# Performance work log

Hardware: AMD Instinct MI355X
Metric: run time of the kernel (lower is better)

Reference implementation:

```python
import jax, jax.numpy as jnp
import numpy as np
from jax import lax

DIM, DIN, NST, DTR, K = 96, 192, 16, 6, 4
B, H, W = 2, 56, 56
MID, SEMID = 24, 24
EPS = 1e-5


def _ln(x, g, b):
    m = x.mean(-1, keepdims=True)
    v = ((x - m) ** 2).mean(-1, keepdims=True)
    return (x - m) / jnp.sqrt(v + EPS) * g + b


def _bn(x, g, b, m, v):  # eval-mode BatchNorm2d, NCHW
    return (x - m[None, :, None, None]) / jnp.sqrt(v[None, :, None, None] + EPS) * g[None, :, None, None] + b[None, :, None, None]


def _conv(x, w, pad, groups=1):
    return lax.conv_general_dilated(x, w, (1, 1), [(pad, pad), (pad, pad)],
                                    dimension_numbers=('NCHW', 'OIHW', 'NCHW'),
                                    feature_group_count=groups)


def _vssm(xn, in_proj_w, conv_w, conv_b, x_proj_w, dt_proj_w, dt_proj_b,
          A_log, Ds, out_norm_g, out_norm_b, out_proj_w):
    Bz, Hh, Ww, C = xn.shape
    L = Hh * Ww
    xz = xn @ in_proj_w.T                      # (B,H,W,2*Din)
    xc, z = jnp.split(xz, 2, axis=-1)
    xc = xc.transpose(0, 3, 1, 2)              # (B,Din,H,W)
    xc = _conv(xc, conv_w, pad=1, groups=DIN) + conv_b[None, :, None, None]
    xc = jax.nn.silu(xc)
    # 4 scan directions: row-major, col-major, and their reverses
    x1 = xc.reshape(Bz, DIN, L)
    x2 = xc.transpose(0, 1, 3, 2).reshape(Bz, DIN, L)
    xs = jnp.stack([x1, x2], axis=1)
    xs = jnp.concatenate([xs, jnp.flip(xs, axis=-1)], axis=1)   # (B,4,Din,L)
    x_dbl = jnp.einsum('bkdl,kcd->bkcl', xs, x_proj_w)          # (B,4,dtR+2N,L)
    dts, Bs, Cs = jnp.split(x_dbl, [DTR, DTR + NST], axis=2)
    delta = jax.nn.softplus(jnp.einsum('bkrl,kdr->bkdl', dts, dt_proj_w)
                            + dt_proj_b[None, :, :, None])      # (B,4,Din,L)
    A = -jnp.exp(A_log).reshape(K, DIN, NST)
    dA = jnp.exp(jnp.einsum('bkdl,kdn->bkdln', delta, A))       # (B,4,Din,L,N)
    dBu = jnp.einsum('bkdl,bknl,bkdl->bkdln', delta, Bs, xs)

    def comb(c1, c2):
        a1, b1 = c1
        a2, b2 = c2
        return (a1 * a2, a2 * b1 + b2)

    _, hs = lax.associative_scan(comb, (dA, dBu), axis=3)       # h_t = dA_t h_{t-1} + dBu_t
    ys = jnp.einsum('bkdln,bknl->bkdl', hs, Cs) + Ds.reshape(1, K, DIN, 1) * xs
    inv = jnp.flip(ys[:, 2:4], axis=-1)

    def t_back(y):
        return y.reshape(Bz, DIN, Ww, Hh).transpose(0, 1, 3, 2).reshape(Bz, DIN, L)

    y = ys[:, 0] + t_back(ys[:, 1]) + inv[:, 0] + t_back(inv[:, 1])
    y = y.reshape(Bz, DIN, Hh, Ww).transpose(0, 2, 3, 1)        # (B,H,W,Din)
    y = _ln(y, out_norm_g, out_norm_b) * jax.nn.silu(z)
    return y @ out_proj_w.T                                      # (B,H,W,dim)


def setup_inputs() -> dict:
    key = jax.random.key(0)
    ks = jax.random.split(key, 16)
    r = lambda k, s, sc=0.05: (jax.random.normal(k, s, dtype=jnp.float32) * sc)
    d = {}
    d['x'] = jax.random.normal(ks[0], (B, DIM, H, W), dtype=jnp.float32)
    d['norm1_g'] = jnp.ones((DIM,), jnp.float32); d['norm1_b'] = jnp.zeros((DIM,), jnp.float32)
    d['in_proj_w'] = r(ks[1], (2 * DIN, DIM))
    d['conv_w'] = r(ks[2], (DIN, 1, 3, 3), 0.2); d['conv_b'] = jnp.zeros((DIN,), jnp.float32)
    d['x_proj_w'] = r(ks[3], (K, DTR + 2 * NST, DIN))
    d['dt_proj_w'] = r(ks[4], (K, DIN, DTR), 0.2)
    d['dt_proj_b'] = jnp.full((K, DIN), -2.0, jnp.float32)
    d['A_log'] = jnp.log(jnp.broadcast_to(jnp.arange(1, NST + 1, dtype=jnp.float32), (K * DIN, NST)) + 0.0)
    d['Ds'] = jnp.ones((K * DIN,), jnp.float32)
    d['out_norm_g'] = jnp.ones((DIN,), jnp.float32); d['out_norm_b'] = jnp.zeros((DIN,), jnp.float32)
    d['out_proj_w'] = r(ks[5], (DIM, DIN))
    d['scale1'] = jnp.full((DIM,), 0.1, jnp.float32)
    d['norm2_g'] = jnp.ones((DIM,), jnp.float32); d['norm2_b'] = jnp.zeros((DIM,), jnp.float32)
    d['lc_w1'] = r(ks[6], (MID, DIM, 1, 1), 0.1)
    d['lc_g1'] = jnp.ones((MID,), jnp.float32); d['lc_b1'] = jnp.zeros((MID,), jnp.float32)
    d['lc_m1'] = jnp.zeros((MID,), jnp.float32); d['lc_v1'] = jnp.ones((MID,), jnp.float32)
    d['lc_w2'] = r(ks[7], (MID, MID, 3, 3), 0.1)
    d['lc_g2'] = jnp.ones((MID,), jnp.float32); d['lc_b2'] = jnp.zeros((MID,), jnp.float32)
    d['lc_m2'] = jnp.zeros((MID,), jnp.float32); d['lc_v2'] = jnp.ones((MID,), jnp.float32)
    d['lc_w3'] = r(ks[8], (DIM, MID, 1, 1), 0.1)
    d['lc_g3'] = jnp.ones((DIM,), jnp.float32); d['lc_b3'] = jnp.zeros((DIM,), jnp.float32)
    d['lc_m3'] = jnp.zeros((DIM,), jnp.float32); d['lc_v3'] = jnp.ones((DIM,), jnp.float32)
    d['se_w1'] = r(ks[9], (SEMID, DIM), 0.1)
    d['se_w2'] = r(ks[10], (DIM, SEMID), 0.1)
    d['scale2'] = jnp.full((DIM,), 0.1, jnp.float32)
    return d


def reference(x, norm1_g, norm1_b, in_proj_w, conv_w, conv_b, x_proj_w, dt_proj_w,
              dt_proj_b, A_log, Ds, out_norm_g, out_norm_b, out_proj_w, scale1,
              norm2_g, norm2_b, lc_w1, lc_g1, lc_b1, lc_m1, lc_v1, lc_w2, lc_g2,
              lc_b2, lc_m2, lc_v2, lc_w3, lc_g3, lc_b3, lc_m3, lc_v3, se_w1,
              se_w2, scale2):
    x_hwc = x.transpose(0, 2, 3, 1)                    # (B,H,W,C)
    vl = _vssm(_ln(x_hwc, norm1_g, norm1_b), in_proj_w, conv_w, conv_b,
               x_proj_w, dt_proj_w, dt_proj_b, A_log, Ds,
               out_norm_g, out_norm_b, out_proj_w)
    vl = vl + scale1 * x_hwc                           # scaled residual
    vb = _ln(vl, norm2_g, norm2_b).transpose(0, 3, 1, 2)  # (B,C,H,W)
    h = jax.nn.relu(_bn(_conv(vb, lc_w1, pad=0), lc_g1, lc_b1, lc_m1, lc_v1))
    h = jax.nn.relu(_bn(_conv(h, lc_w2, pad=1), lc_g2, lc_b2, lc_m2, lc_v2))
    h = _bn(_conv(h, lc_w3, pad=0), lc_g3, lc_b3, lc_m3, lc_v3)
    # SE channel attention
    w = h.mean(axis=(2, 3))                            # (B,C)
    w = jax.nn.sigmoid(jax.nn.relu(w @ se_w1.T) @ se_w2.T)
    h = h * w[:, :, None, None]
    return h + scale2[None, :, None, None] * vl.transpose(0, 3, 1, 2)
```

## Files before the change

kernel.cpp:

```cpp
#include <hip/hip_runtime.h>
#include <math.h>

#define DIMC 96
#define DINC 192
#define NSTC 16
#define DTRC 6
#define KDIR 4
#define BB   2
#define HH   56
#define WWD  56
#define LL   3136
#define NPIX (BB*LL)
#define EPSF 1e-5f
#define NCH  98
#define LC   32
#define NCHAIN (BB*KDIR*DINC)
#define NCOLS 152

#define OFF_XCRAW  0u
#define OFF_XCONV  1204224u
#define OFF_ZS     2408448u
#define OFF_DTS    3612672u
#define OFF_BCB    3763200u
#define OFF_BCC    4164608u
#define OFF_XSCANT 4566016u
#define OFF_CUMD   6974464u
#define OFF_YS     11791360u
#define OFF_HENDT  0u
#define OFF_SUMDT  16608256u
#define OFF_VL     6974464u
#define OFF_H1     7576576u
#define OFF_H2     7727104u
#define OFF_H3     7877632u
#define OFF_POOL   8479744u
#define OFF_SEW    8479936u

__device__ __forceinline__ float siluf(float x) { return x / (1.f + __expf(-x)); }
__device__ __forceinline__ float softplusf(float x) {
    return fmaxf(x, 0.f) + __logf(1.f + __expf(-fabsf(x)));
}
__device__ __forceinline__ float fexp2(float x) {
#if __has_builtin(__builtin_amdgcn_exp2f)
    return __builtin_amdgcn_exp2f(x);
#else
    return exp2f(x);
#endif
}
#define LOG2E 1.44269504088896f

__global__ __launch_bounds__(256) void gemm1_k(const float* __restrict__ x,
                                               const float* __restrict__ g,
                                               const float* __restrict__ bt,
                                               const float* __restrict__ W,
                                               float* __restrict__ xcr,
                                               float* __restrict__ zs) {
    __shared__ float xT[64 * 97];
    __shared__ float wT[96 * 100];
    __shared__ float mA[64], iA[64];
    int row0 = blockIdx.x * 64;
    int b = row0 / LL, pos0 = row0 % LL;
    int c0 = blockIdx.y * 96;
    for (int f = threadIdx.x; f < 96 * 16; f += 256) {
        int ch = f >> 4, po = (f & 15) * 4;
        float4 v = *(const float4*)&x[((size_t)b * DIMC + ch) * LL + pos0 + po];
        xT[(po + 0) * 97 + ch] = v.x; xT[(po + 1) * 97 + ch] = v.y;
        xT[(po + 2) * 97 + ch] = v.z; xT[(po + 3) * 97 + ch] = v.w;
    }
    for (int f = threadIdx.x; f < 96 * 24; f += 256) {
        int r = f / 24, kq = (f % 24) * 4;
        *(float4*)&wT[r * 100 + kq] = *(const float4*)&W[(size_t)(c0 + r) * DIMC + kq];
    }
    __syncthreads();
    if (threadIdx.x < 64) {
        float s = 0.f, q = 0.f;
        const float* xr = &xT[threadIdx.x * 97];
        for (int c = 0; c < 96; ++c) { float v = xr[c]; s += v; q = fmaf(v, v, q); }
        float m = s * (1.f / 96.f);
        mA[threadIdx.x] = m;
        iA[threadIdx.x] = rsqrtf(q * (1.f / 96.f) - m * m + EPSF);
    }
    __syncthreads();
    for (int e = threadIdx.x; e < 64 * 96; e += 256) {
        int row = e / 96, col = e - row * 96;
        float v = xT[row * 97 + col];
        xT[row * 97 + col] = (v - mA[row]) * iA[row] * g[col] + bt[col];
    }
    __syncthreads();
    int tc = threadIdx.x & 15, tr = threadIdx.x >> 4;
    float acc[4][6] = {};
    for (int k = 0; k < 96; ++k) {
        float xv[4], wv[6];
#pragma unroll
        for (int i = 0; i < 4; ++i) xv[i] = xT[(4 * tr + i) * 97 + k];
#pragma unroll
        for (int j = 0; j < 6; ++j) wv[j] = wT[(tc + 16 * j) * 100 + k];
#pragma unroll
        for (int i = 0; i < 4; ++i)
#pragma unroll
            for (int j = 0; j < 6; ++j) acc[i][j] = fmaf(xv[i], wv[j], acc[i][j]);
    }
    int pos = pos0 + 4 * tr;
    if (c0 < DINC) {
#pragma unroll
        for (int j = 0; j < 6; ++j) {
            int col = c0 + tc + 16 * j;
            float4 v = make_float4(acc[0][j], acc[1][j], acc[2][j], acc[3][j]);
            *(float4*)&xcr[((size_t)b * DINC + col) * LL + pos] = v;
        }
    } else {
#pragma unroll
        for (int i = 0; i < 4; ++i)
#pragma unroll
            for (int j = 0; j < 6; ++j) {
                int zc = c0 - DINC + tc + 16 * j;
                zs[(size_t)(row0 + 4 * tr + i) * DINC + zc] = siluf(acc[i][j]);
            }
    }
}

__global__ __launch_bounds__(448) void dwconv_k(const float* __restrict__ xcr,
                                                const float* __restrict__ cw,
                                                const float* __restrict__ cb,
                                                float* __restrict__ xconv) {
    __shared__ float P[56 * 57];
    int bd = blockIdx.x;
    int d = bd % DINC;
    size_t base = (size_t)bd * LL;
    for (int t = threadIdx.x; t < LL; t += 448)
        P[(t / 56) * 57 + (t % 56)] = xcr[base + t];
    float wk[9];
#pragma unroll
    for (int q = 0; q < 9; ++q) wk[q] = cw[d * 9 + q];
    float bias = cb[d];
    __syncthreads();
    for (int t = threadIdx.x; t < LL; t += 448) {
        int h = t / 56, w = t % 56;
        float acc = bias;
#pragma unroll
        for (int ky = 0; ky < 3; ++ky) {
            int y = h + ky - 1;
            if ((unsigned)y >= 56u) continue;
#pragma unroll
            for (int kx = 0; kx < 3; ++kx) {
                int xq = w + kx - 1;
                if ((unsigned)xq >= 56u) continue;
                acc = fmaf(wk[ky * 3 + kx], P[y * 57 + xq], acc);
            }
        }
        xconv[base + t] = siluf(acc);
    }
}

__global__ __launch_bounds__(256) void gemmx_k(const float* __restrict__ xconv,
                                               const float* __restrict__ xpw,
                                               float* __restrict__ dts,
                                               float* __restrict__ bcB,
                                               float* __restrict__ bcC,
                                               float* __restrict__ xscanT) {
    __shared__ float xT[32 * 49];
    __shared__ float wT[38 * 52];
    int row0 = blockIdx.x * 32;
    int b = row0 / LL, pos0 = row0 % LL;
    int by = blockIdx.y;
    int m = threadIdx.x & 31, cg = threadIdx.x >> 5;
    float acc[5] = {};
    for (int kc = 0; kc < 4; ++kc) {
        if (kc) __syncthreads();
        for (int f = threadIdx.x; f < 48 * 8; f += 256) {
            int dd = f >> 3, po = (f & 7) * 4;
            float4 v = *(const float4*)&xconv[((size_t)b * DINC + kc * 48 + dd) * LL + pos0 + po];
            xT[(po + 0) * 49 + dd] = v.x; xT[(po + 1) * 49 + dd] = v.y;
            xT[(po + 2) * 49 + dd] = v.z; xT[(po + 3) * 49 + dd] = v.w;
        }
        for (int f = threadIdx.x; f < 38 * 12; f += 256) {
            int r = f / 12, kq = (f % 12) * 4;
            *(float4*)&wT[r * 52 + kq] =
                *(const float4*)&xpw[(size_t)(by * 38 + r) * DINC + kc * 48 + kq];
        }
        __syncthreads();
#pragma unroll 4
        for (int k = 0; k < 48; ++k) {
            float xv = xT[m * 49 + k];
#pragma unroll
            for (int j = 0; j < 5; ++j) {
                int idx = cg + 8 * j;
                float wv = (idx < 38) ? wT[idx * 52 + k] : 0.f;
                acc[j] = fmaf(xv, wv, acc[j]);
            }
        }
        if (by == 0) {
            for (int f = threadIdx.x; f < 32 * 48; f += 256) {
                int i = f / 48, dd = f - 48 * (f / 48);
                float v = xT[i * 49 + dd];
                int pos = pos0 + i;
                int hh = pos / 56, w = pos - 56 * hh;
                int lt = w * 56 + hh;
                size_t bb = (size_t)b * 2;
                int col = kc * 48 + dd;
                xscanT[(bb * LL + pos) * DINC + col] = v;
                xscanT[((bb + 1) * LL + lt) * DINC + col] = v;
            }
        }
    }
    {
        int pos = pos0 + m;
        int h = pos / 56, w = pos - 56 * h;
        int lt = w * 56 + h;
        int l = (by == 0) ? pos : (by == 1) ? lt : (by == 2) ? (LL - 1 - pos) : (LL - 1 - lt);
        size_t rb = (size_t)(b * KDIR + by) * LL + l;
#pragma unroll
        for (int j = 0; j < 5; ++j) {
            int idx = cg + 8 * j;
            if (idx >= 38) continue;
            float v = acc[j];
            if (idx < DTRC)    dts[rb * DTRC + idx] = v;
            else if (idx < 22) bcB[rb * NSTC + (idx - 6)] = v;
            else               bcC[rb * NSTC + (idx - 22)] = v;
        }
    }
}

__global__ __launch_bounds__(64) void pass1_k(const float* __restrict__ dts,
                                              const float* __restrict__ bcB,
                                              const float* __restrict__ bcC,
                                              const float* __restrict__ alog,
                                              const float* __restrict__ dtw,
                                              const float* __restrict__ dtb,
                                              const float* __restrict__ xscanT,
                                              float* __restrict__ hendT,
                                              float* __restrict__ sumdT,
                                              float* __restrict__ ysT,
                                              float* __restrict__ cumdT) {
    __shared__ float sdt[LC * 7];
    __shared__ float sB[LC * 16];
    __shared__ float sC[LC * 16];
    int blk = blockIdx.x;
    int c = blk % NCH;
    int dtile = (blk / NCH) % 3;
    int bk = blk / (NCH * 3);
    int k = bk & 3, b = bk >> 2;
    int l0 = c * LC;
    int t = threadIdx.x;
    int d = dtile * 64 + t;
    const float* dsrc = dts + ((size_t)bk * LL + l0) * DTRC;
    for (int f = t; f < LC * DTRC; f += 64) sdt[(f / DTRC) * 7 + (f % DTRC)] = dsrc[f];
    const float* bB = bcB + ((size_t)bk * LL + l0) * NSTC;
    const float* bC = bcC + ((size_t)bk * LL + l0) * NSTC;
    for (int f = t; f < LC * NSTC; f += 64) { sB[f] = bB[f]; sC[f] = bC[f]; }
    float wr[DTRC];
    {
        const float* wp = dtw + ((size_t)k * DINC + d) * DTRC;
#pragma unroll
        for (int r = 0; r < DTRC; ++r) wr[r] = wp[r];
    }
    float bias = dtb[k * DINC + d];
    float An2[NSTC];
    {
        const float* ap = alog + ((size_t)(k * DINC + d)) * NSTC;
#pragma unroll
        for (int n = 0; n < NSTC; ++n) An2[n] = -__expf(ap[n]) * LOG2E;
    }
    __syncthreads();
    float h[NSTC];
#pragma unroll
    for (int n = 0; n < NSTC; ++n) h[n] = 0.f;
    float cum = 0.f;
    bool rev = (k >= 2);
    const float* xbase = xscanT + ((size_t)(b * 2 + (k & 1)) * LL) * DINC + d;
    int xi0 = rev ? (LL - 1 - l0) : l0;
    float* yrow = ysT + ((size_t)bk * LL + l0) * DINC + d;
    float* crow = cumdT + ((size_t)bk * LL + l0) * DINC + d;
#pragma unroll 8
    for (int s = 0; s < LC; ++s) {
        float acc = bias;
#pragma unroll
        for (int r = 0; r < DTRC; ++r) acc = fmaf(wr[r], sdt[s * 7 + r], acc);
        float dv = softplusf(acc);
        float xv = xbase[(size_t)(rev ? (xi0 - s) : (xi0 + s)) * DINC];
        cum += dv;
        float dx = dv * xv;
        const float4* B4 = (const float4*)&sB[s * 16];
        const float4* C4 = (const float4*)&sC[s * 16];
        float y = 0.f;
#pragma unroll
        for (int nq = 0; nq < 4; ++nq) {
            float4 Bv = B4[nq], Cv = C4[nq];
            float e0 = fexp2(An2[nq * 4 + 0] * dv);
            h[nq * 4 + 0] = fmaf(e0, h[nq * 4 + 0], dx * Bv.x);
            y = fmaf(h[nq * 4 + 0], Cv.x, y);
            float e1 = fexp2(An2[nq * 4 + 1] * dv);
            h[nq * 4 + 1] = fmaf(e1, h[nq * 4 + 1], dx * Bv.y);
            y = fmaf(h[nq * 4 + 1], Cv.y, y);
            float e2 = fexp2(An2[nq * 4 + 2] * dv);
            h[nq * 4 + 2] = fmaf(e2, h[nq * 4 + 2], dx * Bv.z);
            y = fmaf(h[nq * 4 + 2], Cv.z, y);
            float e3 = fexp2(An2[nq * 4 + 3] * dv);
            h[nq * 4 + 3] = fmaf(e3, h[nq * 4 + 3], dx * Bv.w);
            y = fmaf(h[nq * 4 + 3], Cv.w, y);
        }
        yrow[(size_t)s * DINC] = y;
        crow[(size_t)s * DINC] = cum;
    }
#pragma unroll
    for (int n = 0; n < NSTC; ++n)
        hendT[((size_t)(bk * NCH + c) * NSTC + n) * DINC + d] = h[n];
    sumdT[(size_t)(bk * NCH + c) * DINC + d] = cum;
}

__global__ __launch_bounds__(256) void scan2_k(float* __restrict__ hendT,
                                               const float* __restrict__ sumdT,
                                               const float* __restrict__ alog) {
    int gid = blockIdx.x * 256 + threadIdx.x;
    int d = gid % DINC;
    int n = (gid / DINC) % NSTC;
    int bk = gid / (DINC * NSTC);
    int k = bk & 3;
    float An2 = -__expf(alog[((size_t)(k * DINC + d)) * NSTC + n]) * LOG2E;
    float h = 0.f;
#pragma unroll 4
    for (int c = 0; c < NCH; ++c) {
        size_t idx = ((size_t)(bk * NCH + c) * NSTC + n) * DINC + d;
        float he = hendT[idx];
        float sd = sumdT[(size_t)(bk * NCH + c) * DINC + d];
        hendT[idx] = h;
        h = fmaf(fexp2(An2 * sd), h, he);
    }
}

__global__ __launch_bounds__(256) void pass2_k(const float* __restrict__ bcC,
                                               const float* __restrict__ alog,
                                               const float* __restrict__ hpreT,
                                               const float* __restrict__ cumdT,
                                               float* __restrict__ ysT) {
    __shared__ float sA2[DINC * 17];
    __shared__ float sH[DINC * 17];
    __shared__ float sC[LC * NSTC];
    int blk = blockIdx.x;
    int c = blk % NCH;
    int bk = blk / NCH;
    int k = bk & 3;
    int l0 = c * LC;
    int tid = threadIdx.x;
    const float* ap = alog + (size_t)k * DINC * NSTC;
    for (int f = tid; f < DINC * NSTC; f += 256) {
        int dq = f / NSTC, n = f % NSTC;
        sA2[dq * 17 + n] = -__expf(ap[f]) * LOG2E;
    }
    for (int f = tid; f < DINC * NSTC; f += 256) {
        int n = f / DINC, dq = f % DINC;
        sH[dq * 17 + n] = hpreT[((size_t)(bk * NCH + c) * NSTC + n) * DINC + dq];
    }
    const float* bC = bcC + ((size_t)bk * LL + l0) * NSTC;
    for (int f = tid; f < LC * NSTC; f += 256) sC[f] = bC[f];
    __syncthreads();
    for (int e = tid; e < LC * DINC; e += 256) {
        int li = e / DINC, d = e - DINC * (e / DINC);
        size_t gq = ((size_t)bk * LL + l0 + li) * DINC + d;
        float cd = cumdT[gq];
        float y = ysT[gq];
        const float* A = &sA2[d * 17];
        const float* Hp = &sH[d * 17];
        const float* Cp = &sC[li * NSTC];
#pragma unroll
        for (int n = 0; n < NSTC; ++n)
            y = fmaf(Hp[n] * fexp2(A[n] * cd), Cp[n], y);
        ysT[gq] = y;
    }
}

__global__ __launch_bounds__(256) void gemm2_k(const float* __restrict__ ysT,
                                               const float* __restrict__ xscanT,
                                               const float* __restrict__ dsv,
                                               const float* __restrict__ g,
                                               const float* __restrict__ bt,
                                               const float* __restrict__ zs,
                                               const float* __restrict__ opw,
                                               const float* __restrict__ x,
                                               const float* __restrict__ sc1,
                                               float* __restrict__ vl) {
    __shared__ float xT[16 * 193];
    __shared__ float wT[96 * 52];
    __shared__ float mA[16], iA[16];
    __shared__ float sD[DINC];
    int row0 = blockIdx.x * 16;
    int b = row0 / LL, pos0 = row0 % LL;
    if (threadIdx.x < DINC)
        sD[threadIdx.x] = dsv[threadIdx.x] + dsv[DINC + threadIdx.x] +
                          dsv[2 * DINC + threadIdx.x] + dsv[3 * DINC + threadIdx.x];
    __syncthreads();
    size_t base = (size_t)b * KDIR * LL;
    size_t xbase = (size_t)b * 2 * LL;
    for (int f = threadIdx.x; f < 16 * DINC; f += 256) {
        int r = f / DINC, d = f - DINC * (f / DINC);
        int pos = pos0 + r;
        int hh = pos / 56, w = pos - 56 * hh;
        int lt = w * 56 + hh;
        float y = ysT[(base + pos) * DINC + d]
                + ysT[(base + LL + lt) * DINC + d]
                + ysT[(base + 2 * LL + (LL - 1 - pos)) * DINC + d]
                + ysT[(base + 3 * LL + (LL - 1 - lt)) * DINC + d];
        float xv = xscanT[(xbase + pos) * DINC + d];
        xT[r * 193 + d] = fmaf(xv, sD[d], y);
    }
    __syncthreads();
    {
        int r = threadIdx.x >> 4, sc = threadIdx.x & 15;
        float s = 0.f, q = 0.f;
#pragma unroll
        for (int j = 0; j < 12; ++j) {
            float v = xT[r * 193 + sc + 16 * j];
            s += v; q = fmaf(v, v, q);
        }
        s += __shfl_xor(s, 1, 16); q += __shfl_xor(q, 1, 16);
        s += __shfl_xor(s, 2, 16); q += __shfl_xor(q, 2, 16);
        s += __shfl_xor(s, 4, 16); q += __shfl_xor(q, 4, 16);
        s += __shfl_xor(s, 8, 16); q += __shfl_xor(q, 8, 16);
        if (sc == 0) {
            float m = s * (1.f / 192.f);
            mA[r] = m;
            iA[r] = rsqrtf(q * (1.f / 192.f) - m * m + EPSF);
        }
    }
    __syncthreads();
    for (int e = threadIdx.x; e < 16 * 192; e += 256) {
        int row = e / 192, col = e - row * 192;
        float v = xT[row * 193 + col];
        float z = zs[(size_t)row0 * DINC + e];
        xT[row * 193 + col] = ((v - mA[row]) * iA[row] * g[col] + bt[col]) * z;
    }
    int tc = threadIdx.x & 15, tr = threadIdx.x >> 4;
    float acc[6] = {};
    for (int kc = 0; kc < 4; ++kc) {
        __syncthreads();
        for (int f = threadIdx.x; f < 96 * 12; f += 256) {
            int r = f / 12, kq = (f % 12) * 4;
            *(float4*)&wT[r * 52 + kq] = *(const float4*)&opw[(size_t)r * DINC + kc * 48 + kq];
        }
        __syncthreads();
#pragma unroll 4
        for (int k = 0; k < 48; ++k) {
            float xv = xT[tr * 193 + kc * 48 + k];
#pragma unroll
            for (int j = 0; j < 6; ++j) acc[j] = fmaf(xv, wT[(tc + 16 * j) * 52 + k], acc[j]);
        }
    }
    {
        int pos = pos0 + tr;
#pragma unroll
        for (int j = 0; j < 6; ++j) {
            int col = tc + 16 * j;
            float v = fmaf(sc1[col], x[((size_t)b * DIMC + col) * LL + pos], acc[j]);
            vl[(size_t)(row0 + tr) * DIMC + col] = v;
        }
    }
}

__global__ __launch_bounds__(256) void ln2conv1_k(const float* __restrict__ vl,
                                                  const float* __restrict__ g,
                                                  const float* __restrict__ bt,
                                                  const float* __restrict__ w1,
                                                  const float* __restrict__ g1,
                                                  const float* __restrict__ b1,
                                                  const float* __restrict__ m1,
                                                  const float* __restrict__ v1,
                                                  float* __restrict__ h1) {
    __shared__ float row[4][96];
    int wv = threadIdx.x >> 6, lane = threadIdx.x & 63;
    int pix = blockIdx.x * 4 + wv;
    const float* vr = vl + (size_t)pix * DIMC;
    float a0 = vr[lane];
    float a1 = (lane < 32) ? vr[64 + lane] : 0.f;
    float s = a0 + a1, q = a0 * a0 + a1 * a1;
    for (int o = 32; o; o >>= 1) { s += __shfl_xor(s, o, 64); q += __shfl_xor(q, o, 64); }
    float m = s * (1.f / 96.f);
    float inv = rsqrtf(q * (1.f / 96.f) - m * m + EPSF);
    row[wv][lane] = (a0 - m) * inv * g[lane] + bt[lane];
    if (lane < 32) row[wv][64 + lane] = (a1 - m) * inv * g[64 + lane] + bt[64 + lane];
    __syncthreads();
    if (lane < 24) {
        const float* wr = w1 + lane * 96;
        float acc = 0.f;
#pragma unroll 8
        for (int c = 0; c < 96; ++c) acc = fmaf(row[wv][c], wr[c], acc);
        float bn = (acc - m1[lane]) * rsqrtf(v1[lane] + EPSF) * g1[lane] + b1[lane];
        int b = pix / LL, pos = pix % LL;
        h1[((size_t)b * 24 + lane) * LL + pos] = fmaxf(bn, 0.f);
    }
}

__global__ __launch_bounds__(256) void conv2_k(const float* __restrict__ h1,
                                               const float* __restrict__ w2,
                                               const float* __restrict__ g2,
                                               const float* __restrict__ b2,
                                               const float* __restrict__ m2,
                                               const float* __restrict__ v2,
                                               float* __restrict__ h2) {
    int i = blockIdx.x * 256 + threadIdx.x;
    int pos = i % LL, mo = (i / LL) % 24, b = i / (LL * 24);
    int hh = pos / WWD, ww = pos % WWD;
    float acc = 0.f;
    for (int c = 0; c < 24; ++c) {
        const float* src = h1 + ((size_t)b * 24 + c) * LL;
        const float* wk = w2 + ((size_t)(mo * 24 + c)) * 9;
#pragma unroll
        for (int ky = 0; ky < 3; ++ky) {
            int y = hh + ky - 1;
            if ((unsigned)y >= HH) continue;
#pragma unroll
            for (int kx = 0; kx < 3; ++kx) {
                int xq = ww + kx - 1;
                if ((unsigned)xq >= WWD) continue;
                acc = fmaf(wk[ky * 3 + kx], src[y * WWD + xq], acc);
            }
        }
    }
    float bn = (acc - m2[mo]) * rsqrtf(v2[mo] + EPSF) * g2[mo] + b2[mo];
    h2[i] = fmaxf(bn, 0.f);
}

__global__ __launch_bounds__(256) void conv3_k(const float* __restrict__ h2,
                                               const float* __restrict__ w3,
                                               const float* __restrict__ g3,
                                               const float* __restrict__ b3,
                                               const float* __restrict__ m3,
                                               const float* __restrict__ v3,
                                               float* __restrict__ h3) {
    int i = blockIdx.x * 256 + threadIdx.x;
    int pos = i % LL, c = (i / LL) % DIMC, b = i / (LL * DIMC);
    const float* wr = w3 + c * 24;
    float acc = 0.f;
#pragma unroll
    for (int mo = 0; mo < 24; ++mo)
        acc = fmaf(wr[mo], h2[((size_t)b * 24 + mo) * LL + pos], acc);
    h3[i] = (acc - m3[c]) * rsqrtf(v3[c] + EPSF) * g3[c] + b3[c];
}

__global__ __launch_bounds__(256) void pool_k(const float* __restrict__ h3,
                                              float* __restrict__ pooled) {
    int bc = blockIdx.x;
    const float* p = h3 + (size_t)bc * LL;
    float s = 0.f;
    for (int i = threadIdx.x; i < LL; i += 256) s += p[i];
    for (int o = 32; o; o >>= 1) s += __shfl_xor(s, o, 64);
    __shared__ float wsum[4];
    if ((threadIdx.x & 63) == 0) wsum[threadIdx.x >> 6] = s;
    __syncthreads();
    if (threadIdx.x == 0) pooled[bc] = (wsum[0] + wsum[1] + wsum[2] + wsum[3]) * (1.f / 3136.f);
}

__global__ __launch_bounds__(128) void semlp_k(const float* __restrict__ pooled,
                                               const float* __restrict__ sw1,
                                               const float* __restrict__ sw2,
                                               float* __restrict__ sew) {
    __shared__ float pl[2][96];
    __shared__ float hid[2][24];
    for (int i = threadIdx.x; i < 192; i += 128) pl[i / 96][i % 96] = pooled[i];
    __syncthreads();
    if (threadIdx.x < 48) {
        int b = threadIdx.x / 24, mo = threadIdx.x % 24;
        float acc = 0.f;
        for (int c = 0; c < 96; ++c) acc = fmaf(pl[b][c], sw1[mo * 96 + c], acc);
        hid[b][mo] = fmaxf(acc, 0.f);
    }
    __syncthreads();
    for (int i = threadIdx.x; i < 192; i += 128) {
        int b = i / 96, c = i % 96;
        float acc = 0.f;
        for (int mo = 0; mo < 24; ++mo) acc = fmaf(hid[b][mo], sw2[c * 24 + mo], acc);
        sew[i] = 1.f / (1.f + __expf(-acc));
    }
}

__global__ __launch_bounds__(256) void final_k(const float* __restrict__ h3,
                                               const float* __restrict__ sew,
                                               const float* __restrict__ vl,
                                               const float* __restrict__ sc2,
                                               float* __restrict__ out) {
    int i = blockIdx.x * 256 + threadIdx.x;
    int pos = i % LL, c = (i / LL) % DIMC, b = i / (LL * DIMC);
    out[i] = fmaf(h3[i], sew[b * DIMC + c],
                  sc2[c] * vl[((size_t)b * LL + pos) * DIMC + c]);
}

extern "C" void kernel_launch(void* const* d_in, const int* in_sizes, int n_in,
                              void* d_out, int out_size, void* d_ws, size_t ws_size,
                              hipStream_t stream) {
    const float* x    = (const float*)d_in[0];
    const float* n1g  = (const float*)d_in[1];
    const float* n1b  = (const float*)d_in[2];
    const float* ipw  = (const float*)d_in[3];
    const float* cw   = (const float*)d_in[4];
    const float* cb   = (const float*)d_in[5];
    const float* xpw  = (const float*)d_in[6];
    const float* dtw  = (const float*)d_in[7];
    const float* dtb  = (const float*)d_in[8];
    const float* alog = (const float*)d_in[9];
    const float* dsv  = (const float*)d_in[10];
    const float* ong  = (const float*)d_in[11];
    const float* onb  = (const float*)d_in[12];
    const float* opw  = (const float*)d_in[13];
    const float* sc1  = (const float*)d_in[14];
    const float* n2g  = (const float*)d_in[15];
    const float* n2b  = (const float*)d_in[16];
    const float* w1   = (const float*)d_in[17];
    const float* g1   = (const float*)d_in[18];
    const float* b1   = (const float*)d_in[19];
    const float* m1   = (const float*)d_in[20];
    const float* v1   = (const float*)d_in[21];
    const float* w2   = (const float*)d_in[22];
    const float* g2   = (const float*)d_in[23];
    const float* b2   = (const float*)d_in[24];
    const float* m2   = (const float*)d_in[25];
    const float* v2   = (const float*)d_in[26];
    const float* w3   = (const float*)d_in[27];
    const float* g3   = (const float*)d_in[28];
    const float* b3   = (const float*)d_in[29];
    const float* m3   = (const float*)d_in[30];
    const float* v3   = (const float*)d_in[31];
    const float* sw1  = (const float*)d_in[32];
    const float* sw2  = (const float*)d_in[33];
    const float* sc2  = (const float*)d_in[34];
    float* ws = (float*)d_ws;
    float* out = (float*)d_out;

    gemm1_k<<<dim3(NPIX / 64, 4), 256, 0, stream>>>(x, n1g, n1b, ipw,
                                                    ws + OFF_XCRAW, ws + OFF_ZS);
    dwconv_k<<<BB * DINC, 448, 0, stream>>>(ws + OFF_XCRAW, cw, cb, ws + OFF_XCONV);
    gemmx_k<<<dim3(NPIX / 32, 4), 256, 0, stream>>>(ws + OFF_XCONV, xpw, ws + OFF_DTS,
                                                    ws + OFF_BCB, ws + OFF_BCC, ws + OFF_XSCANT);

    pass1_k<<<BB * KDIR * 3 * NCH, 64, 0, stream>>>(
        ws + OFF_DTS, ws + OFF_BCB, ws + OFF_BCC, alog, dtw, dtb,
        ws + OFF_XSCANT, ws + OFF_HENDT, ws + OFF_SUMDT, ws + OFF_YS, ws + OFF_CUMD);
    scan2_k<<<(NCHAIN * NSTC) / 256, 256, 0, stream>>>(ws + OFF_HENDT, ws + OFF_SUMDT, alog);
    pass2_k<<<BB * KDIR * NCH, 256, 0, stream>>>(
        ws + OFF_BCC, alog, ws + OFF_HENDT, ws + OFF_CUMD, ws + OFF_YS);

    gemm2_k<<<NPIX / 16, 256, 0, stream>>>(ws + OFF_YS, ws + OFF_XSCANT, dsv,
                                           ong, onb, ws + OFF_ZS, opw, x, sc1, ws + OFF_VL);
    ln2conv1_k<<<NPIX / 4, 256, 0, stream>>>(ws + OFF_VL, n2g, n2b, w1, g1, b1, m1, v1,
                                             ws + OFF_H1);
    conv2_k<<<(BB * 24 * LL) / 256, 256, 0, stream>>>(ws + OFF_H1, w2, g2, b2, m2, v2,
                                                      ws + OFF_H2);
    conv3_k<<<(BB * DIMC * LL) / 256, 256, 0, stream>>>(ws + OFF_H2, w3, g3, b3, m3, v3,
                                                        ws + OFF_H3);
    pool_k<<<BB * DIMC, 256, 0, stream>>>(ws + OFF_H3, ws + OFF_POOL);
    semlp_k<<<1, 128, 0, stream>>>(ws + OFF_POOL, sw1, sw2, ws + OFF_SEW);
    final_k<<<(BB * DIMC * LL) / 256, 256, 0, stream>>>(ws + OFF_H3, ws + OFF_SEW, ws + OFF_VL,
                                                        sc2, out);
    (void)in_sizes; (void)n_in; (void)out_size; (void)ws_size;
}
```

Before: 218.6 us.

## Halve scan chunk length and retile in_proj GEMM to 32-row blocks

Changes the selective-scan chunking from 98 chunks of 32 to 196 chunks of 16 and moves the chunk-end state buffers to new workspace offsets. The first GEMM now processes 32 rows per block with one row per thread and 12 output columns, does the LayerNorm statistics with all threads plus shuffle reductions, and stages the z output through shared memory so its global writes are coalesced. The aim is more parallelism in the scan and fewer serial steps per chunk, plus better load balance and coalescing in the GEMM. The cost is more chunk-boundary state traffic, a longer inter-chunk carry scan, and a GEMM with less register-level reuse of loaded operands.

```diff
diff --git a/kernel.cpp b/kernel.cpp
--- a/kernel.cpp
+++ b/kernel.cpp
@@ -12,8 +12,8 @@
 #define LL   3136
 #define NPIX (BB*LL)
 #define EPSF 1e-5f
-#define NCH  98
-#define LC   32
+#define NCH  196
+#define LC   16
 #define NCHAIN (BB*KDIR*DINC)
 #define NCOLS 152
 
@@ -26,8 +26,8 @@
 #define OFF_XSCANT 4566016u
 #define OFF_CUMD   6974464u
 #define OFF_YS     11791360u
-#define OFF_HENDT  0u
-#define OFF_SUMDT  16608256u
+#define OFF_HENDT  16608256u
+#define OFF_SUMDT  21425152u
 #define OFF_VL     6974464u
 #define OFF_H1     7576576u
 #define OFF_H2     7727104u
@@ -54,14 +54,15 @@
                                                const float* __restrict__ W,
                                                float* __restrict__ xcr,
                                                float* __restrict__ zs) {
-    __shared__ float xT[64 * 97];
+    __shared__ float xT[32 * 97];
     __shared__ float wT[96 * 100];
-    __shared__ float mA[64], iA[64];
-    int row0 = blockIdx.x * 64;
+    __shared__ float mA[32], iA[32];
+    int row0 = blockIdx.x * 32;
     int b = row0 / LL, pos0 = row0 % LL;
-    int c0 = blockIdx.y * 96;
-    for (int f = threadIdx.x; f < 96 * 16; f += 256) {
-        int ch = f >> 4, po = (f & 15) * 4;
+    int by = blockIdx.y;
+    int c0 = by * 96;
+    for (int f = threadIdx.x; f < 96 * 8; f += 256) {
+        int ch = f >> 3, po = (f & 7) * 4;
         float4 v = *(const float4*)&x[((size_t)b * DIMC + ch) * LL + pos0 + po];
         xT[(po + 0) * 97 + ch] = v.x; xT[(po + 1) * 97 + ch] = v.y;
         xT[(po + 2) * 97 + ch] = v.z; xT[(po + 3) * 97 + ch] = v.w;
@@ -71,50 +72,53 @@
         *(float4*)&wT[r * 100 + kq] = *(const float4*)&W[(size_t)(c0 + r) * DIMC + kq];
     }
     __syncthreads();
-    if (threadIdx.x < 64) {
+    {
+        int r = threadIdx.x >> 3, sc = threadIdx.x & 7;
         float s = 0.f, q = 0.f;
-        const float* xr = &xT[threadIdx.x * 97];
-        for (int c = 0; c < 96; ++c) { float v = xr[c]; s += v; q = fmaf(v, v, q); }
-        float m = s * (1.f / 96.f);
-        mA[threadIdx.x] = m;
-        iA[threadIdx.x] = rsqrtf(q * (1.f / 96.f) - m * m + EPSF);
-    }
-    __syncthreads();
-    for (int e = threadIdx.x; e < 64 * 96; e += 256) {
+#pragma unroll
+        for (int j = 0; j < 12; ++j) {
+            float v = xT[r * 97 + sc + 8 * j];
+            s += v; q = fmaf(v, v, q);
+        }
+        s += __shfl_xor(s, 1, 8); q += __shfl_xor(q, 1, 8);
+        s += __shfl_xor(s, 2, 8); q += __shfl_xor(q, 2, 8);
+        s += __shfl_xor(s, 4, 8); q += __shfl_xor(q, 4, 8);
+        if (sc == 0) {
+            float m = s * (1.f / 96.f);
+            mA[r] = m;
+            iA[r] = rsqrtf(q * (1.f / 96.f) - m * m + EPSF);
+        }
+    }
+    __syncthreads();
+    for (int e = threadIdx.x; e < 32 * 96; e += 256) {
         int row = e / 96, col = e - row * 96;
         float v = xT[row * 97 + col];
         xT[row * 97 + col] = (v - mA[row]) * iA[row] * g[col] + bt[col];
     }
     __syncthreads();
-    int tc = threadIdx.x & 15, tr = threadIdx.x >> 4;
-    float acc[4][6] = {};
+    int m = threadIdx.x & 31, cg = threadIdx.x >> 5;
+    float acc[12] = {};
     for (int k = 0; k < 96; ++k) {
-        float xv[4], wv[6];
-#pragma unroll
-        for (int i = 0; i < 4; ++i) xv[i] = xT[(4 * tr + i) * 97 + k];
-#pragma unroll
-        for (int j = 0; j < 6; ++j) wv[j] = wT[(tc + 16 * j) * 100 + k];
-#pragma unroll
-        for (int i = 0; i < 4; ++i)
-#pragma unroll
-            for (int j = 0; j < 6; ++j) acc[i][j] = fmaf(xv[i], wv[j], acc[i][j]);
-    }
-    int pos = pos0 + 4 * tr;
+        float xv = xT[m * 97 + k];
+#pragma unroll
+        for (int j = 0; j < 12; ++j) acc[j] = fmaf(xv, wT[(cg + 8 * j) * 100 + k], acc[j]);
+    }
     if (c0 < DINC) {
 #pragma unroll
-        for (int j = 0; j < 6; ++j) {
-            int col = c0 + tc + 16 * j;
-            float4 v = make_float4(acc[0][j], acc[1][j], acc[2][j], acc[3][j]);
-            *(float4*)&xcr[((size_t)b * DINC + col) * LL + pos] = v;
+        for (int j = 0; j < 12; ++j) {
+            int col = c0 + cg + 8 * j;
+            xcr[((size_t)b * DINC + col) * LL + pos0 + m] = acc[j];
         }
     } else {
-#pragma unroll
-        for (int i = 0; i < 4; ++i)
-#pragma unroll
-            for (int j = 0; j < 6; ++j) {
-                int zc = c0 - DINC + tc + 16 * j;
-                zs[(size_t)(row0 + 4 * tr + i) * DINC + zc] = siluf(acc[i][j]);
-            }
+        __syncthreads();
+#pragma unroll
+        for (int j = 0; j < 12; ++j) xT[m * 97 + cg + 8 * j] = acc[j];
+        __syncthreads();
+        int zoff = (by - 2) * 96;
+        for (int e = threadIdx.x; e < 32 * 96; e += 256) {
+            int r = e / 96, cq = e - 96 * (e / 96);
+            zs[(size_t)(row0 + r) * DINC + zoff + cq] = siluf(xT[r * 97 + cq]);
+        }
     }
 }
 
@@ -623,7 +627,7 @@
     float* ws = (float*)d_ws;
     float* out = (float*)d_out;
 
-    gemm1_k<<<dim3(NPIX / 64, 4), 256, 0, stream>>>(x, n1g, n1b, ipw,
+    gemm1_k<<<dim3(NPIX / 32, 4), 256, 0, stream>>>(x, n1g, n1b, ipw,
                                                     ws + OFF_XCRAW, ws + OFF_ZS);
     dwconv_k<<<BB * DINC, 448, 0, stream>>>(ws + OFF_XCRAW, cw, cb, ws + OFF_XCONV);
     gemmx_k<<<dim3(NPIX / 32, 4), 256, 0, stream>>>(ws + OFF_XCONV, xpw, ws + OFF_DTS,
```

New measurement: 241.5 us. +10.4%, slower.
